# Kernel optimization log

Hardware: AMD Instinct MI355X
Metric: run time of the kernel (lower is better)

The kernel has to match this reference:

```python
import jax, jax.numpy as jnp
import numpy as np

B, T, D, H, L, W = 32, 512, 256, 8, 2, 10
NQ = 10000
HD = D // H


def setup_inputs():
    key = jax.random.key(0)
    ks = jax.random.split(key, 16)
    def n(k, shape, s=0.02):
        return jax.random.normal(k, shape, jnp.float32) * s
    return {
        "q": jax.random.randint(ks[0], (B, T), 0, NQ),
        "s": jax.random.randint(ks[1], (B, T), 0, 2),
        "q_embed": n(ks[2], (NQ + 1, D)),
        "s_embed": n(ks[3], (2, D)),
        "pos_embed": n(ks[4], (512, D)),
        "fusion_w": n(ks[5], (2 * D, D)),
        "fusion_b": jnp.zeros((D,), jnp.float32),
        "in_proj_w": n(ks[6], (L, D, 3 * D)),
        "in_proj_b": jnp.zeros((L, 3 * D), jnp.float32),
        "out_proj_w": n(ks[7], (L, D, D)),
        "out_proj_b": jnp.zeros((L, D), jnp.float32),
        "ln1_g": jnp.ones((L, D), jnp.float32),
        "ln1_b": jnp.zeros((L, D), jnp.float32),
        "ln2_g": jnp.ones((L, D), jnp.float32),
        "ln2_b": jnp.zeros((L, D), jnp.float32),
        "ff1_w": n(ks[8], (L, D, 4 * D)),
        "ff1_b": jnp.zeros((L, 4 * D), jnp.float32),
        "ff2_w": n(ks[9], (L, 4 * D, D)),
        "ff2_b": jnp.zeros((L, D), jnp.float32),
        "sw1": n(ks[10], (6, 32), 0.1),
        "sb1": jnp.zeros((32,), jnp.float32),
        "sw2": n(ks[11], (32, D // 4), 0.1),
        "sb2": jnp.zeros((D // 4,), jnp.float32),
        "cw1": n(ks[12], (D + D // 4, D)),
        "cb1": jnp.zeros((D,), jnp.float32),
        "cw2": n(ks[13], (D, 1)),
        "cb2": jnp.zeros((1,), jnp.float32),
    }


def _ln(x, g, b):
    mu = jnp.mean(x, -1, keepdims=True)
    var = jnp.mean(jnp.square(x - mu), -1, keepdims=True)
    return (x - mu) * jax.lax.rsqrt(var + 1e-5) * g + b


def _sliding_sum(x, w):
    # sum over trailing window of size w ending at each t, via prefix sums
    c = jnp.concatenate([jnp.zeros((x.shape[0], 1), x.dtype), jnp.cumsum(x, axis=1)], axis=1)
    t = jnp.arange(x.shape[1])
    return c[:, t + 1] - c[:, jnp.maximum(t + 1 - w, 0)]


def _stats(s, mask):
    # vectorized version of _extract_statistics (prefix-sum sliding windows)
    mf = mask.astype(jnp.float32)
    sf = s.astype(jnp.float32) * mf
    valid = _sliding_sum(mf, W)
    correct_rate = _sliding_sum(sf, W) / (valid + 1e-6)
    rc = _sliding_sum(mf, 5)
    recent_correct = _sliding_sum(sf, 5) / (rc + 1e-6)
    trans = ((s[:, 1:] != s[:, :-1]) & mask[:, 1:] & mask[:, :-1]).astype(jnp.float32)
    diff = jnp.concatenate([jnp.zeros((s.shape[0], 1), jnp.float32), trans], axis=1)
    change_rate = _sliding_sum(diff, W - 1) / (valid + 1e-6)
    # max consecutive equal run within each trailing window of size W
    sp = jnp.pad(s, ((0, 0), (W - 1, 0)))
    mp = jnp.pad(mask, ((0, 0), (W - 1, 0)))
    win_s = [sp[:, j:j + T] for j in range(W)]
    win_m = [mp[:, j:j + T] for j in range(W)]
    run = win_m[0].astype(jnp.float32)
    mx = run
    for j in range(1, W):  # fixed small window, not a data-dim loop
        eq = (win_s[j] == win_s[j - 1]) & win_m[j - 1]
        run = win_m[j].astype(jnp.float32) * (jnp.where(eq, run, 0.0) + 1.0)
        mx = jnp.maximum(mx, run)
    rel = jnp.broadcast_to(jnp.arange(T, dtype=jnp.float32) / max(T, 100), s.shape)
    cov = valid / W
    return jnp.stack([correct_rate, recent_correct, change_rate, mx / W, rel, cov], axis=-1)


def reference(q, s, q_embed, s_embed, pos_embed, fusion_w, fusion_b, in_proj_w, in_proj_b,
              out_proj_w, out_proj_b, ln1_g, ln1_b, ln2_g, ln2_b, ff1_w, ff1_b, ff2_w, ff2_b,
              sw1, sb1, sw2, sb2, cw1, cb1, cw2, cb2):
    mask = s >= 0
    qm = jnp.where(mask, q, 0)
    sm = jnp.where(mask, s, 0)
    h = jnp.concatenate([q_embed[qm], s_embed[sm]], axis=-1)  # [B,T,2D]
    h = jax.nn.relu(h @ fusion_w + fusion_b) + pos_embed[:T][None]
    causal = jnp.tril(jnp.ones((T, T), bool))
    allowed = causal[None, None] & mask[:, None, None, :]
    scale = 1.0 / (HD ** 0.5)
    for l in range(L):
        qkv = h @ in_proj_w[l] + in_proj_b[l]
        qh, kh, vh = jnp.split(qkv, 3, axis=-1)
        qh = qh.reshape(B, T, H, HD).transpose(0, 2, 1, 3)
        kh = kh.reshape(B, T, H, HD).transpose(0, 2, 1, 3)
        vh = vh.reshape(B, T, H, HD).transpose(0, 2, 1, 3)
        scores = jnp.einsum('bhqd,bhkd->bhqk', qh, kh) * scale
        scores = jnp.where(allowed, scores, -1e9)
        attn = jax.nn.softmax(scores, axis=-1)
        o = jnp.einsum('bhqk,bhkd->bhqd', attn, vh).transpose(0, 2, 1, 3).reshape(B, T, D)
        h = _ln(h + (o @ out_proj_w[l] + out_proj_b[l]), ln1_g[l], ln1_b[l])
        ff = jax.nn.gelu(h @ ff1_w[l] + ff1_b[l], approximate=False) @ ff2_w[l] + ff2_b[l]
        h = _ln(h + ff, ln2_g[l], ln2_b[l])
    sfeat = _stats(sm, mask)  # [B,T,6]
    semb = jax.nn.relu(sfeat @ sw1 + sb1) @ sw2 + sb2  # [B,T,D//4]
    comb = jnp.concatenate([h, semb], axis=-1)
    logits = (jax.nn.relu(comb @ cw1 + cb1) @ cw2 + cb2)[..., 0]
    return jnp.where(mask, logits, -1e9)
```

## Files before the change

kernel.cpp:

```cpp
#include <hip/hip_runtime.h>
#include <hip/hip_bf16.h>
#include <cmath>


using short8 = __attribute__((ext_vector_type(8))) short;
using short4v = __attribute__((ext_vector_type(4))) short;
using f32x4  = __attribute__((ext_vector_type(4))) float;

__device__ inline float gelu_f(float x) {
    return 0.5f * x * (1.0f + erff(x * 0.70710678118654752f));
}

__device__ inline short f2bf(float x) {
    union { float f; unsigned u; } v; v.f = x;
    return (short)((v.u + 0x7fffu + ((v.u >> 16) & 1u)) >> 16);
}

__device__ inline float bf2f(short v) {
    union { unsigned u; float f; } x; x.u = ((unsigned)(unsigned short)v) << 16;
    return x.f;
}

__device__ inline unsigned packbf(float lo, float hi) {
    union { float f; unsigned u; } a, b; a.f = lo; b.f = hi;
    unsigned ra = (a.u + 0x7fffu + ((a.u >> 16) & 1u)) >> 16;
    unsigned rb = (b.u + 0x7fffu + ((b.u >> 16) & 1u)) >> 16;
    return (rb << 16) | (ra & 0xffffu);
}

#define GLOAD16(gp, lp) __builtin_amdgcn_global_load_lds( \
    (const __attribute__((address_space(1))) void*)(gp), \
    (__attribute__((address_space(3))) void*)(lp), 16, 0, 0)

__global__ __launch_bounds__(256) void prep(
    const float* __restrict__ fusion_w, const float* __restrict__ in_proj_w,
    const float* __restrict__ out_proj_w, const float* __restrict__ ff1_w,
    const float* __restrict__ ff2_w, const float* __restrict__ cw1,
    short* __restrict__ wts,
    const int* __restrict__ s,
    short* __restrict__ semb,
    const float* __restrict__ sw1, const float* __restrict__ sb1,
    const float* __restrict__ sw2, const float* __restrict__ sb2)
{
    __shared__ float tile[32][33];
    __shared__ float sv_sh[512];
    __shared__ float m_sh[512];
    __shared__ float sw2_sh[2048];

    if (blockIdx.x < 1744) {
        const int b0[10]      = {0,128,320,512,576,640,896,1152,1408,1664};
        const int Ks[10]      = {512,256,256,256,256,256,256,1024,1024,320};
        const int Ns[10]      = {256,768,768,256,256,1024,1024,256,256,256};
        const int sidx[10]    = {0,1,1,2,2,3,3,4,4,5};
        const size_t soff[10] = {0,0,196608,0,65536,0,262144,0,262144,0};
        const size_t doff[10] = {0,131072,327680,524288,589824,655360,917504,1179648,1441792,1703936};
        const float* srcs[6] = {fusion_w, in_proj_w, out_proj_w, ff1_w, ff2_w, cw1};
        int bid = blockIdx.x;
        int mi = 0;
        while (mi < 9 && bid >= b0[mi + 1]) ++mi;
        int bl = bid - b0[mi];
        int K = Ks[mi], N = Ns[mi];
        int tx = bl % (N >> 5), ty = bl / (N >> 5);
        const float* src = srcs[sidx[mi]] + soff[mi];
        short* dst = wts + doff[mi];
        int c = threadIdx.x & 31, r = threadIdx.x >> 5;
#pragma unroll
        for (int i = 0; i < 4; ++i)
            tile[r + i * 8][c] = src[(size_t)(ty * 32 + r + i * 8) * N + tx * 32 + c];
        __syncthreads();
#pragma unroll
        for (int i = 0; i < 4; ++i)
            dst[(size_t)(tx * 32 + r + i * 8) * K + ty * 32 + c] = f2bf(tile[c][r + i * 8]);
    } else {
        const int b = blockIdx.x - 1744;
        const int tt = threadIdx.x;
        for (int t = tt; t < 512; t += 256) {
            int sval = s[b * 512 + t];
            bool mk = sval >= 0;
            sv_sh[t] = mk ? (float)sval : 0.f;
            m_sh[t] = mk ? 1.f : 0.f;
        }
        for (int i = tt; i < 2048; i += 256) sw2_sh[i] = sw2[i];
        __syncthreads();
        for (int half = 0; half < 2; ++half) {
            const int t = tt + half * 256;
            float mf10 = 0, sf10 = 0, mf5 = 0, sf5 = 0, d9 = 0;
#pragma unroll
            for (int k = 0; k < 10; ++k) {
                int idx = t - k;
                if (idx >= 0) {
                    float mv = m_sh[idx], sv = sv_sh[idx];
                    mf10 += mv; sf10 += sv;
                    if (k < 5) { mf5 += mv; sf5 += sv; }
                    if (k < 9 && idx >= 1) {
                        if (sv != sv_sh[idx - 1] && mv > 0.5f && m_sh[idx - 1] > 0.5f) d9 += 1.f;
                    }
                }
            }
            float run, mx;
            {
                int x0 = t - 9;
                run = (x0 >= 0) ? m_sh[x0] : 0.f;
                mx = run;
#pragma unroll
                for (int j = 1; j < 10; ++j) {
                    int xc = t + j - 9, xp = xc - 1;
                    float sc = (xc >= 0) ? sv_sh[xc] : 0.f;
                    float sp = (xp >= 0) ? sv_sh[xp] : 0.f;
                    float mc = (xc >= 0) ? m_sh[xc] : 0.f;
                    float mp = (xp >= 0) ? m_sh[xp] : 0.f;
                    bool eq = (sc == sp) && (mp > 0.5f);
                    run = (mc > 0.5f) ? ((eq ? run : 0.f) + 1.f) : 0.f;
                    mx = fmaxf(mx, run);
                }
            }
            float f[6];
            f[0] = sf10 / (mf10 + 1e-6f);
            f[1] = sf5 / (mf5 + 1e-6f);
            f[2] = d9 / (mf10 + 1e-6f);
            f[3] = mx * 0.1f;
            f[4] = (float)t * (1.f / 512.f);
            f[5] = mf10 * 0.1f;

            float hid[32];
#pragma unroll
            for (int j2 = 0; j2 < 32; ++j2) {
                float a = sb1[j2];
#pragma unroll
                for (int i = 0; i < 6; ++i) a = fmaf(f[i], sw1[i * 32 + j2], a);
                hid[j2] = fmaxf(a, 0.f);
            }
            short* orow = semb + ((size_t)b * 512 + t) * 64;
            for (int c = 0; c < 64; c += 4) {
                float v0 = sb2[c], v1 = sb2[c + 1], v2 = sb2[c + 2], v3 = sb2[c + 3];
#pragma unroll
                for (int j2 = 0; j2 < 32; ++j2) {
                    float hh = hid[j2];
                    v0 = fmaf(hh, sw2_sh[j2 * 64 + c], v0);
                    v1 = fmaf(hh, sw2_sh[j2 * 64 + c + 1], v1);
                    v2 = fmaf(hh, sw2_sh[j2 * 64 + c + 2], v2);
                    v3 = fmaf(hh, sw2_sh[j2 * 64 + c + 3], v3);
                }
                short4v o; o[0] = f2bf(v0); o[1] = f2bf(v1); o[2] = f2bf(v2); o[3] = f2bf(v3);
                *(short4v*)(orow + c) = o;
            }
        }
    }
}

template<int EPI, int KTOT>
__global__ __launch_bounds__(512) void kbs(
    const short* __restrict__ A, const short* __restrict__ Wt,
    const float* __restrict__ bias,
    short* __restrict__ o0, short* __restrict__ o1, short* __restrict__ o2,
    const float* __restrict__ pos,
    const int* __restrict__ qi, const int* __restrict__ si,
    const float* __restrict__ qe, const float* __restrict__ se)
{
    constexpr int BN = 64;
    constexpr int NCH = (KTOT + 255) / 256;
    __shared__ short Bs[BN * 256];
    const int tid = threadIdx.x, lane = tid & 63, wv = tid >> 6;
    const int lg = lane >> 4, lr = lane & 15;
    const int n0 = blockIdx.y * BN;
    const int row0 = blockIdx.x * 128 + wv * 16;

    f32x4 acc[4] = {};
    short8 af[8];

#pragma unroll
    for (int c = 0; c < NCH; ++c) {
        const int ck = (KTOT - c * 256 >= 256) ? 256 : (KTOT - c * 256);
        const int spr = ck >> 3;
        if (c) __syncthreads();
        for (int i = 0; i < (BN * ck) / 8; i += 512) {
            int slot = i + tid;
            int n = slot / spr, posn = slot % spr;
            int g = posn ^ (n & 7);
            GLOAD16(Wt + (size_t)(n0 + n) * KTOT + c * 256 + g * 8, &Bs[slot * 8]);
        }
        const int nkk = ck >> 5;
        if constexpr (EPI == 0) {
            int row = row0 + lr;
            int sv = si[row];
            bool mk = sv >= 0;
            const float* base = (c == 0) ? qe + (size_t)(mk ? qi[row] : 0) * 256
                                         : se + (size_t)(mk ? sv : 0) * 256;
#pragma unroll
            for (int kk = 0; kk < 8; ++kk) {
                const float* p = base + kk * 32 + lg * 8;
                float4 v0 = *(const float4*)p;
                float4 v1 = *(const float4*)(p + 4);
                short8 o;
                o[0] = f2bf(v0.x); o[1] = f2bf(v0.y); o[2] = f2bf(v0.z); o[3] = f2bf(v0.w);
                o[4] = f2bf(v1.x); o[5] = f2bf(v1.y); o[6] = f2bf(v1.z); o[7] = f2bf(v1.w);
                af[kk] = o;
            }
        } else {
            const short* ar = A + (size_t)(row0 + lr) * KTOT + c * 256 + lg * 8;
#pragma unroll
            for (int kk = 0; kk < 8; ++kk)
                if (kk < nkk) af[kk] = *(const short8*)(ar + kk * 32);
        }
        __syncthreads();
#pragma unroll
        for (int kk = 0; kk < 8; ++kk) {
            if (kk >= nkk) break;
#pragma unroll
            for (int j = 0; j < 4; ++j) {
                int n = j * 16 + lr;
                short8 b = *(const short8*)&Bs[n * ck + (((kk * 4 + lg) ^ (n & 7)) << 3)];
                acc[j] = __builtin_amdgcn_mfma_f32_16x16x32_bf16(af[kk], b, acc[j], 0, 0, 0);
            }
        }
    }

    if constexpr (EPI == 0) {
#pragma unroll
        for (int j = 0; j < 4; ++j)
#pragma unroll
        for (int r = 0; r < 4; ++r) {
            int row = row0 + lg * 4 + r;
            int col = n0 + j * 16 + lr;
            float x = acc[j][r] + bias[col];
            x = fmaxf(x, 0.f) + pos[(size_t)(row & 511) * 256 + col];
            o0[(size_t)row * 256 + col] = f2bf(x);
        }
    } else if constexpr (EPI == 1) {
#pragma unroll
        for (int j = 0; j < 4; ++j)
#pragma unroll
        for (int r = 0; r < 4; ++r) {
            int row = row0 + lg * 4 + r;
            int gcol = n0 + j * 16 + lr;
            int t = row & 511, bg = row >> 9;
            int sec = gcol >> 8, cc = gcol & 255;
            int h = cc >> 5, d = cc & 31, bh = bg * 8 + h;
            short v = f2bf(acc[j][r] + bias[gcol]);
            if (sec == 0)      o0[((size_t)bh * 512 + t) * 32 + d] = v;
            else if (sec == 1) o1[((size_t)bh * 512 + t) * 32 + d] = v;
            else {
                int kl = t & 31;
                o2[(size_t)bh * 16384 + (size_t)(t >> 5) * 1024 +
                   (size_t)((kl >> 2) & 3) * 256 + d * 8 + (((kl & 3) << 1) | ((kl >> 4) & 1))] = v;
            }
        }
    } else {
#pragma unroll
        for (int j = 0; j < 4; ++j)
#pragma unroll
        for (int r = 0; r < 4; ++r) {
            int row = row0 + lg * 4 + r;
            int gcol = n0 + j * 16 + lr;
            float x = acc[j][r] + bias[gcol];
            o0[(size_t)row * 1024 + gcol] = f2bf(gelu_f(x));
        }
    }
}

template<int EPI, int KTOT>
__global__ __launch_bounds__(512) void kfull(
    const short* __restrict__ A, const short* __restrict__ A2,
    const short* __restrict__ Wt, const float* __restrict__ bias,
    short* __restrict__ hb,
    const float* __restrict__ gamma, const float* __restrict__ beta,
    const float* __restrict__ cw2v, const float* __restrict__ cb2,
    const int* __restrict__ smask, float* __restrict__ outlog)
{
    constexpr int NCH = (KTOT + 127) / 128;
    constexpr int KA = (EPI == 1) ? 256 : KTOT;
    __shared__ short Bs[256 * 128];
    __shared__ float redS[32][4];
    __shared__ float redQ[32][4];
    const int tid = threadIdx.x, lane = tid & 63, wv = tid >> 6;
    const int lg = lane >> 4, lr = lane & 15;
    const int wr = wv >> 2, wc = wv & 3;
    const int row0 = blockIdx.x * 32 + wr * 16;

    f32x4 acc[4] = {};
    short8 af[4];

#pragma unroll
    for (int c = 0; c < NCH; ++c) {
        const int ck = (KTOT - c * 128 >= 128) ? 128 : (KTOT - c * 128);
        const int spr = ck >> 3;
        if (c) __syncthreads();
        for (int i = 0; i < (256 * ck) / 8; i += 512) {
            int slot = i + tid;
            int n = slot / spr, posn = slot % spr;
            int g = posn ^ (n & 7);
            GLOAD16(Wt + (size_t)n * KTOT + c * 128 + g * 8, &Bs[slot * 8]);
        }
        const int nkk = ck >> 5;
        if (EPI == 1 && c == 2) {
            const short* ar2 = A2 + (size_t)(row0 + lr) * 64 + lg * 8;
            af[0] = *(const short8*)(ar2);
            af[1] = *(const short8*)(ar2 + 32);
        } else {
            const short* ar = A + (size_t)(row0 + lr) * KA + c * 128 + lg * 8;
#pragma unroll
            for (int kk = 0; kk < 4; ++kk)
                if (kk < nkk) af[kk] = *(const short8*)(ar + kk * 32);
        }
        __syncthreads();
#pragma unroll
        for (int kk = 0; kk < 4; ++kk) {
            if (kk >= nkk) break;
#pragma unroll
            for (int j = 0; j < 4; ++j) {
                int n = wc * 64 + j * 16 + lr;
                short8 b = *(const short8*)&Bs[n * ck + (((kk * 4 + lg) ^ (n & 7)) << 3)];
                acc[j] = __builtin_amdgcn_mfma_f32_16x16x32_bf16(af[kk], b, acc[j], 0, 0, 0);
            }
        }
    }

    if constexpr (EPI == 0) {
        float ps[4] = {0.f, 0.f, 0.f, 0.f}, pq[4] = {0.f, 0.f, 0.f, 0.f};
#pragma unroll
        for (int j = 0; j < 4; ++j)
#pragma unroll
        for (int r = 0; r < 4; ++r) {
            int row = row0 + lg * 4 + r;
            int col = wc * 64 + j * 16 + lr;
            float x = acc[j][r] + bias[col] + bf2f(hb[(size_t)row * 256 + col]);
            acc[j][r] = x;
            ps[r] += x; pq[r] += x * x;
        }
#pragma unroll
        for (int off = 1; off < 16; off <<= 1)
#pragma unroll
            for (int r = 0; r < 4; ++r) {
                ps[r] += __shfl_xor(ps[r], off);
                pq[r] += __shfl_xor(pq[r], off);
            }
        if (lr == 0) {
#pragma unroll
            for (int r = 0; r < 4; ++r) {
                int rl = wr * 16 + lg * 4 + r;
                redS[rl][wc] = ps[r]; redQ[rl][wc] = pq[r];
            }
        }
        __syncthreads();
#pragma unroll
        for (int r = 0; r < 4; ++r) {
            int rl = wr * 16 + lg * 4 + r;
            int row = row0 + lg * 4 + r;
            float sm = redS[rl][0] + redS[rl][1] + redS[rl][2] + redS[rl][3];
            float sq = redQ[rl][0] + redQ[rl][1] + redQ[rl][2] + redQ[rl][3];
            float mu = sm * (1.f / 256.f);
            float var = sq * (1.f / 256.f) - mu * mu;
            float rstd = rsqrtf(var + 1e-5f);
#pragma unroll
            for (int j = 0; j < 4; ++j) {
                int col = wc * 64 + j * 16 + lr;
                float y = (acc[j][r] - mu) * rstd * gamma[col] + beta[col];
                hb[(size_t)row * 256 + col] = f2bf(y);
            }
        }
    } else {
        float p[4] = {0.f, 0.f, 0.f, 0.f};
#pragma unroll
        for (int j = 0; j < 4; ++j)
#pragma unroll
        for (int r = 0; r < 4; ++r) {
            int col = wc * 64 + j * 16 + lr;
            float v = fmaxf(acc[j][r] + bias[col], 0.f);
            p[r] += v * cw2v[col];
        }
#pragma unroll
        for (int off = 1; off < 16; off <<= 1)
#pragma unroll
            for (int r = 0; r < 4; ++r) p[r] += __shfl_xor(p[r], off);
        if (lr == 0) {
#pragma unroll
            for (int r = 0; r < 4; ++r)
                redS[wr * 16 + lg * 4 + r][wc] = p[r];
        }
        __syncthreads();
        if (tid < 32) {
            int row = blockIdx.x * 32 + tid;
            float v = redS[tid][0] + redS[tid][1] + redS[tid][2] + redS[tid][3] + cb2[0];
            outlog[row] = (smask[row] >= 0) ? v : -1e9f;
        }
    }
}

__global__ __launch_bounds__(256) void attn_mfma(
    const short* __restrict__ Qg, const short* __restrict__ Kg,
    const short* __restrict__ VTg, short* __restrict__ O)
{
    __shared__ unsigned Wp[4][2][16][20];
    const int bh = blockIdx.x >> 2, part = blockIdx.x & 3;
    const int b = bh >> 3, h = bh & 7;
    const int wv = threadIdx.x >> 6, lane = threadIdx.x & 63;
    const int lg = lane >> 4, lr = lane & 15;
    const int slot = part * 4 + wv;
    const short* Qbh = Qg + (size_t)bh * 16384;
    const short* Kbh = Kg + (size_t)bh * 16384;
    const short* Vbh = VTg + (size_t)bh * 16384;
    const float scale = 0.17677669529663687f;

    const int tA = slot, tB = 31 - slot;
    const int qA0 = tA << 4, qB0 = tB << 4;
    const int nA = tA >> 1, nB = tB >> 1;
    short8 qaA = *(const short8*)(Qbh + (size_t)(qA0 + lr) * 32 + lg * 8);
    short8 qaB = *(const short8*)(Qbh + (size_t)(qB0 + lr) * 32 + lg * 8);
    f32x4 oA0 = {}, oA1 = {}, oB0 = {}, oB1 = {};
    float lA[4] = {0.f, 0.f, 0.f, 0.f};
    float lB[4] = {0.f, 0.f, 0.f, 0.f};

    auto chunk = [&](int c, int q0, int nfull, const short8& qa,
                     const short8& kf0, const short8& kf1,
                     const short8& vf0, const short8& vf1,
                     f32x4& o0, f32x4& o1, float* l_, int slab) {
        int kc = c << 5;
        f32x4 s0 = {}, s1 = {};
        s0 = __builtin_amdgcn_mfma_f32_16x16x32_bf16(qa, kf0, s0, 0, 0, 0);
        s1 = __builtin_amdgcn_mfma_f32_16x16x32_bf16(qa, kf1, s1, 0, 0, 0);
        float p0[4], p1[4];
        if (c < nfull) {
#pragma unroll
            for (int r = 0; r < 4; ++r) {
                p0[r] = __expf(s0[r] * scale);
                p1[r] = __expf(s1[r] * scale);
            }
        } else {
#pragma unroll
            for (int r = 0; r < 4; ++r) {
                int qq = q0 + lg * 4 + r;
                p0[r] = (kc + lr)      > qq ? 0.f : __expf(s0[r] * scale);
                p1[r] = (kc + 16 + lr) > qq ? 0.f : __expf(s1[r] * scale);
            }
        }
#pragma unroll
        for (int r = 0; r < 4; ++r) {
            l_[r] += p0[r] + p1[r];
            Wp[wv][slab][lg * 4 + r][lr] = packbf(p0[r], p1[r]);
        }
        short8 pa = *(const short8*)&Wp[wv][slab][lr][lg * 4];
        o0 = __builtin_amdgcn_mfma_f32_16x16x32_bf16(pa, vf0, o0, 0, 0, 0);
        o1 = __builtin_amdgcn_mfma_f32_16x16x32_bf16(pa, vf1, o1, 0, 0, 0);
    };

    int c = 0;
    for (; c <= nA; ++c) {
        int kc = c << 5;
        short8 kf0 = *(const short8*)(Kbh + (size_t)(kc + lr) * 32 + lg * 8);
        short8 kf1 = *(const short8*)(Kbh + (size_t)(kc + 16 + lr) * 32 + lg * 8);
        short8 vf0 = *(const short8*)(Vbh + (size_t)c * 1024 + lg * 256 + lr * 8);
        short8 vf1 = *(const short8*)(Vbh + (size_t)c * 1024 + lg * 256 + (lr + 16) * 8);
        chunk(c, qB0, nB, qaB, kf0, kf1, vf0, vf1, oB0, oB1, lB, 1);
        chunk(c, qA0, nA, qaA, kf0, kf1, vf0, vf1, oA0, oA1, lA, 0);
    }
    for (; c <= nB; ++c) {
        int kc = c << 5;
        short8 kf0 = *(const short8*)(Kbh + (size_t)(kc + lr) * 32 + lg * 8);
        short8 kf1 = *(const short8*)(Kbh + (size_t)(kc + 16 + lr) * 32 + lg * 8);
        short8 vf0 = *(const short8*)(Vbh + (size_t)c * 1024 + lg * 256 + lr * 8);
        short8 vf1 = *(const short8*)(Vbh + (size_t)c * 1024 + lg * 256 + (lr + 16) * 8);
        chunk(c, qB0, nB, qaB, kf0, kf1, vf0, vf1, oB0, oB1, lB, 1);
    }

#pragma unroll
    for (int off = 1; off < 16; off <<= 1)
#pragma unroll
        for (int r = 0; r < 4; ++r) {
            lA[r] += __shfl_xor(lA[r], off);
            lB[r] += __shfl_xor(lB[r], off);
        }
#pragma unroll
    for (int r = 0; r < 4; ++r) {
        float invA = 1.f / lA[r];
        size_t roA = ((size_t)b * 512 + qA0 + lg * 4 + r) * 256 + h * 32;
        O[roA + lr] = f2bf(oA0[r] * invA);
        O[roA + 16 + lr] = f2bf(oA1[r] * invA);
        float invB = 1.f / lB[r];
        size_t roB = ((size_t)b * 512 + qB0 + lg * 4 + r) * 256 + h * 32;
        O[roB + lr] = f2bf(oB0[r] * invB);
        O[roB + 16 + lr] = f2bf(oB1[r] * invB);
    }
}

extern "C" void kernel_launch(void* const* d_in, const int* in_sizes, int n_in,
                              void* d_out, int out_size, void* d_ws, size_t ws_size,
                              hipStream_t stream) {
    const int*   q         = (const int*)d_in[0];
    const int*   s         = (const int*)d_in[1];
    const float* q_embed   = (const float*)d_in[2];
    const float* s_embed   = (const float*)d_in[3];
    const float* pos_embed = (const float*)d_in[4];
    const float* fusion_w  = (const float*)d_in[5];
    const float* fusion_b  = (const float*)d_in[6];
    const float* in_proj_w = (const float*)d_in[7];
    const float* in_proj_b = (const float*)d_in[8];
    const float* out_proj_w= (const float*)d_in[9];
    const float* out_proj_b= (const float*)d_in[10];
    const float* ln1_g     = (const float*)d_in[11];
    const float* ln1_b     = (const float*)d_in[12];
    const float* ln2_g     = (const float*)d_in[13];
    const float* ln2_b     = (const float*)d_in[14];
    const float* ff1_w     = (const float*)d_in[15];
    const float* ff1_b     = (const float*)d_in[16];
    const float* ff2_w     = (const float*)d_in[17];
    const float* ff2_b     = (const float*)d_in[18];
    const float* sw1       = (const float*)d_in[19];
    const float* sb1       = (const float*)d_in[20];
    const float* sw2       = (const float*)d_in[21];
    const float* sb2       = (const float*)d_in[22];
    const float* cw1       = (const float*)d_in[23];
    const float* cb1       = (const float*)d_in[24];
    const float* cw2       = (const float*)d_in[25];
    const float* cb2       = (const float*)d_in[26];
    float* out = (float*)d_out;

    char* base = (char*)d_ws;
    short* hb   = (short*)(base);
    short* bufA = (short*)(base + 8388608);
    short* att  = (short*)(base + 41943040);
    short* Qg   = (short*)(base + 50331648);
    short* Kg   = (short*)(base + 58720256);
    short* VTg  = (short*)(base + 67108864);
    short* semb = (short*)(base + 75497472);
    short* wts  = (short*)(base + 77594624);

    const size_t W_FUSION = 0, W_INPROJ0 = 131072, W_INPROJ1 = 327680;
    const size_t W_OUTPROJ0 = 524288, W_OUTPROJ1 = 589824;
    const size_t W_FF1_0 = 655360, W_FF1_1 = 917504;
    const size_t W_FF2_0 = 1179648, W_FF2_1 = 1441792;
    const size_t W_CW1 = 1703936;

    prep<<<1776, 256, 0, stream>>>(fusion_w, in_proj_w, out_proj_w,
                                   ff1_w, ff2_w, cw1, wts,
                                   s, semb, sw1, sb1, sw2, sb2);
    kbs<0, 512><<<dim3(128, 4), 512, 0, stream>>>(nullptr,
        wts + W_FUSION, fusion_b, hb, nullptr, nullptr,
        pos_embed, q, s, q_embed, s_embed);
    for (int l = 0; l < 2; ++l) {
        kbs<1, 256><<<dim3(128, 12), 512, 0, stream>>>(hb,
            wts + (l ? W_INPROJ1 : W_INPROJ0), in_proj_b + l * 768,
            Qg, Kg, VTg, nullptr, nullptr, nullptr, nullptr, nullptr);
        attn_mfma<<<1024, 256, 0, stream>>>(Qg, Kg, VTg, att);
        kfull<0, 256><<<512, 512, 0, stream>>>(att, nullptr,
            wts + (l ? W_OUTPROJ1 : W_OUTPROJ0), out_proj_b + l * 256,
            hb, ln1_g + l * 256, ln1_b + l * 256,
            nullptr, nullptr, nullptr, nullptr);
        kbs<2, 256><<<dim3(128, 16), 512, 0, stream>>>(hb,
            wts + (l ? W_FF1_1 : W_FF1_0), ff1_b + l * 1024,
            bufA, nullptr, nullptr, nullptr, nullptr, nullptr, nullptr, nullptr);
        kfull<0, 1024><<<512, 512, 0, stream>>>(bufA, nullptr,
            wts + (l ? W_FF2_1 : W_FF2_0), ff2_b + l * 256,
            hb, ln2_g + l * 256, ln2_b + l * 256,
            nullptr, nullptr, nullptr, nullptr);
    }
    kfull<1, 320><<<512, 512, 0, stream>>>(hb, semb,
        wts + W_CW1, cb1, nullptr, nullptr, nullptr,
        cw2, cb2, s, out);
}
```

Measured before the change: 280.8 us.

## Reuse weight tile across multiple M sub-tiles and double-buffer attention P staging

The kbs GEMM now loads the full-K weight slice into LDS once and loops over MS row sub-tiles, halving the grid for the QKV and FF1 projections. This amortises the weight loads across more rows, at the cost of larger LDS use (64xKTOT, which is 64 KB for the 512-wide fusion GEMM) and fewer blocks. In attention, exp is switched to exp2 with a prescaled log2e constant, and the P staging buffer is split by chunk parity to reduce the write-after-read hazard between iterations.

New measurement: 290.3 us. 3.4% more time.

```diff
diff --git a/kernel.cpp b/kernel.cpp
--- a/kernel.cpp
+++ b/kernel.cpp
@@ -148,7 +148,7 @@
     }
 }
 
-template<int EPI, int KTOT>
+template<int EPI, int KTOT, int MS>
 __global__ __launch_bounds__(512) void kbs(
     const short* __restrict__ A, const short* __restrict__ Wt,
     const float* __restrict__ bias,
@@ -158,37 +158,35 @@
     const float* __restrict__ qe, const float* __restrict__ se)
 {
     constexpr int BN = 64;
-    constexpr int NCH = (KTOT + 255) / 256;
-    __shared__ short Bs[BN * 256];
+    constexpr int SPR = KTOT / 8;
+    constexpr int NK = KTOT / 32;
+    __shared__ short Bs[BN * KTOT];
     const int tid = threadIdx.x, lane = tid & 63, wv = tid >> 6;
     const int lg = lane >> 4, lr = lane & 15;
     const int n0 = blockIdx.y * BN;
-    const int row0 = blockIdx.x * 128 + wv * 16;
-
-    f32x4 acc[4] = {};
-    short8 af[8];
-
-#pragma unroll
-    for (int c = 0; c < NCH; ++c) {
-        const int ck = (KTOT - c * 256 >= 256) ? 256 : (KTOT - c * 256);
-        const int spr = ck >> 3;
-        if (c) __syncthreads();
-        for (int i = 0; i < (BN * ck) / 8; i += 512) {
-            int slot = i + tid;
-            int n = slot / spr, posn = slot % spr;
-            int g = posn ^ (n & 7);
-            GLOAD16(Wt + (size_t)(n0 + n) * KTOT + c * 256 + g * 8, &Bs[slot * 8]);
-        }
-        const int nkk = ck >> 5;
+
+#pragma unroll
+    for (int i = 0; i < (BN * SPR) / 512; ++i) {
+        int slot = i * 512 + tid;
+        int n = slot / SPR, posn = slot % SPR;
+        int g = posn ^ (n & 7);
+        GLOAD16(Wt + (size_t)(n0 + n) * KTOT + g * 8, &Bs[slot * 8]);
+    }
+    __syncthreads();
+
+#pragma unroll
+    for (int m = 0; m < MS; ++m) {
+        const int row0 = (blockIdx.x * MS + m) * 128 + wv * 16;
+        short8 af[NK];
         if constexpr (EPI == 0) {
             int row = row0 + lr;
             int sv = si[row];
             bool mk = sv >= 0;
-            const float* base = (c == 0) ? qe + (size_t)(mk ? qi[row] : 0) * 256
-                                         : se + (size_t)(mk ? sv : 0) * 256;
-#pragma unroll
-            for (int kk = 0; kk < 8; ++kk) {
-                const float* p = base + kk * 32 + lg * 8;
+            const float* b0 = qe + (size_t)(mk ? qi[row] : 0) * 256;
+            const float* b1 = se + (size_t)(mk ? sv : 0) * 256;
+#pragma unroll
+            for (int kk = 0; kk < NK; ++kk) {
+                const float* p = ((kk < 8) ? b0 + kk * 32 : b1 + (kk - 8) * 32) + lg * 8;
                 float4 v0 = *(const float4*)p;
                 float4 v1 = *(const float4*)(p + 4);
                 short8 o;
@@ -197,63 +195,63 @@
                 af[kk] = o;
             }
         } else {
-            const short* ar = A + (size_t)(row0 + lr) * KTOT + c * 256 + lg * 8;
-#pragma unroll
-            for (int kk = 0; kk < 8; ++kk)
-                if (kk < nkk) af[kk] = *(const short8*)(ar + kk * 32);
-        }
-        __syncthreads();
-#pragma unroll
-        for (int kk = 0; kk < 8; ++kk) {
-            if (kk >= nkk) break;
+            const short* ar = A + (size_t)(row0 + lr) * KTOT + lg * 8;
+#pragma unroll
+            for (int kk = 0; kk < NK; ++kk)
+                af[kk] = *(const short8*)(ar + kk * 32);
+        }
+
+        f32x4 acc[4] = {};
+#pragma unroll
+        for (int kk = 0; kk < NK; ++kk) {
 #pragma unroll
             for (int j = 0; j < 4; ++j) {
                 int n = j * 16 + lr;
-                short8 b = *(const short8*)&Bs[n * ck + (((kk * 4 + lg) ^ (n & 7)) << 3)];
+                short8 b = *(const short8*)&Bs[n * KTOT + (((kk * 4 + lg) ^ (n & 7)) << 3)];
                 acc[j] = __builtin_amdgcn_mfma_f32_16x16x32_bf16(af[kk], b, acc[j], 0, 0, 0);
             }
         }
-    }
-
-    if constexpr (EPI == 0) {
-#pragma unroll
-        for (int j = 0; j < 4; ++j)
-#pragma unroll
-        for (int r = 0; r < 4; ++r) {
-            int row = row0 + lg * 4 + r;
-            int col = n0 + j * 16 + lr;
-            float x = acc[j][r] + bias[col];
-            x = fmaxf(x, 0.f) + pos[(size_t)(row & 511) * 256 + col];
-            o0[(size_t)row * 256 + col] = f2bf(x);
-        }
-    } else if constexpr (EPI == 1) {
-#pragma unroll
-        for (int j = 0; j < 4; ++j)
-#pragma unroll
-        for (int r = 0; r < 4; ++r) {
-            int row = row0 + lg * 4 + r;
-            int gcol = n0 + j * 16 + lr;
-            int t = row & 511, bg = row >> 9;
-            int sec = gcol >> 8, cc = gcol & 255;
-            int h = cc >> 5, d = cc & 31, bh = bg * 8 + h;
-            short v = f2bf(acc[j][r] + bias[gcol]);
-            if (sec == 0)      o0[((size_t)bh * 512 + t) * 32 + d] = v;
-            else if (sec == 1) o1[((size_t)bh * 512 + t) * 32 + d] = v;
-            else {
-                int kl = t & 31;
-                o2[(size_t)bh * 16384 + (size_t)(t >> 5) * 1024 +
-                   (size_t)((kl >> 2) & 3) * 256 + d * 8 + (((kl & 3) << 1) | ((kl >> 4) & 1))] = v;
-            }
-        }
-    } else {
-#pragma unroll
-        for (int j = 0; j < 4; ++j)
-#pragma unroll
-        for (int r = 0; r < 4; ++r) {
-            int row = row0 + lg * 4 + r;
-            int gcol = n0 + j * 16 + lr;
-            float x = acc[j][r] + bias[gcol];
-            o0[(size_t)row * 1024 + gcol] = f2bf(gelu_f(x));
+
+        if constexpr (EPI == 0) {
+#pragma unroll
+            for (int j = 0; j < 4; ++j)
+#pragma unroll
+            for (int r = 0; r < 4; ++r) {
+                int row = row0 + lg * 4 + r;
+                int col = n0 + j * 16 + lr;
+                float x = acc[j][r] + bias[col];
+                x = fmaxf(x, 0.f) + pos[(size_t)(row & 511) * 256 + col];
+                o0[(size_t)row * 256 + col] = f2bf(x);
+            }
+        } else if constexpr (EPI == 1) {
+#pragma unroll
+            for (int j = 0; j < 4; ++j)
+#pragma unroll
+            for (int r = 0; r < 4; ++r) {
+                int row = row0 + lg * 4 + r;
+                int gcol = n0 + j * 16 + lr;
+                int t = row & 511, bg = row >> 9;
+                int sec = gcol >> 8, cc = gcol & 255;
+                int h = cc >> 5, d = cc & 31, bh = bg * 8 + h;
+                short v = f2bf(acc[j][r] + bias[gcol]);
+                if (sec == 0)      o0[((size_t)bh * 512 + t) * 32 + d] = v;
+                else if (sec == 1) o1[((size_t)bh * 512 + t) * 32 + d] = v;
+                else {
+                    int kl = t & 31;
+                    o2[(size_t)bh * 16384 + (size_t)(t >> 5) * 1024 +
+                       (size_t)((kl >> 2) & 3) * 256 + d * 8 + (((kl & 3) << 1) | ((kl >> 4) & 1))] = v;
+                }
+            }
+        } else {
+#pragma unroll
+            for (int j = 0; j < 4; ++j)
+#pragma unroll
+            for (int r = 0; r < 4; ++r) {
+                int row = row0 + lg * 4 + r;
+                int gcol = n0 + j * 16 + lr;
+                float x = acc[j][r] + bias[gcol];
+                o0[(size_t)row * 1024 + gcol] = f2bf(gelu_f(x));
+            }
         }
     }
 }
@@ -390,7 +388,7 @@
     const short* __restrict__ Qg, const short* __restrict__ Kg,
     const short* __restrict__ VTg, short* __restrict__ O)
 {
-    __shared__ unsigned Wp[4][2][16][20];
+    __shared__ unsigned Wp[4][2][2][16][20];
     const int bh = blockIdx.x >> 2, part = blockIdx.x & 3;
     const int b = bh >> 3, h = bh & 7;
     const int wv = threadIdx.x >> 6, lane = threadIdx.x & 63;
@@ -399,7 +397,7 @@
     const short* Qbh = Qg + (size_t)bh * 16384;
     const short* Kbh = Kg + (size_t)bh * 16384;
     const short* Vbh = VTg + (size_t)bh * 16384;
-    const float scale = 0.17677669529663687f;
+    const float cs = 0.25503590f;
 
     const int tA = slot, tB = 31 - slot;
     const int qA0 = tA << 4, qB0 = tB << 4;
@@ -415,6 +413,7 @@
                      const short8& vf0, const short8& vf1,
                      f32x4& o0, f32x4& o1, float* l_, int slab) {
         int kc = c << 5;
+        int par = c & 1;
         f32x4 s0 = {}, s1 = {};
         s0 = __builtin_amdgcn_mfma_f32_16x16x32_bf16(qa, kf0, s0, 0, 0, 0);
         s1 = __builtin_amdgcn_mfma_f32_16x16x32_bf16(qa, kf1, s1, 0, 0, 0);
@@ -422,23 +421,23 @@
         if (c < nfull) {
 #pragma unroll
             for (int r = 0; r < 4; ++r) {
-                p0[r] = __expf(s0[r] * scale);
-                p1[r] = __expf(s1[r] * scale);
+                p0[r] = exp2f(s0[r] * cs);
+                p1[r] = exp2f(s1[r] * cs);
             }
         } else {
 #pragma unroll
             for (int r = 0; r < 4; ++r) {
                 int qq = q0 + lg * 4 + r;
-                p0[r] = (kc + lr)      > qq ? 0.f : __expf(s0[r] * scale);
-                p1[r] = (kc + 16 + lr) > qq ? 0.f : __expf(s1[r] * scale);
+                p0[r] = (kc + lr)      > qq ? 0.f : exp2f(s0[r] * cs);
+                p1[r] = (kc + 16 + lr) > qq ? 0.f : exp2f(s1[r] * cs);
             }
         }
 #pragma unroll
         for (int r = 0; r < 4; ++r) {
             l_[r] += p0[r] + p1[r];
-            Wp[wv][slab][lg * 4 + r][lr] = packbf(p0[r], p1[r]);
-        }
-        short8 pa = *(const short8*)&Wp[wv][slab][lr][lg * 4];
+            Wp[wv][slab][par][lg * 4 + r][lr] = packbf(p0[r], p1[r]);
+        }
+        short8 pa = *(const short8*)&Wp[wv][slab][par][lr][lg * 4];
         o0 = __builtin_amdgcn_mfma_f32_16x16x32_bf16(pa, vf0, o0, 0, 0, 0);
         o1 = __builtin_amdgcn_mfma_f32_16x16x32_bf16(pa, vf1, o1, 0, 0, 0);
     };
@@ -533,11 +532,11 @@
     prep<<<1776, 256, 0, stream>>>(fusion_w, in_proj_w, out_proj_w,
                                    ff1_w, ff2_w, cw1, wts,
                                    s, semb, sw1, sb1, sw2, sb2);
-    kbs<0, 512><<<dim3(128, 4), 512, 0, stream>>>(nullptr,
+    kbs<0, 512, 1><<<dim3(128, 4), 512, 0, stream>>>(nullptr,
         wts + W_FUSION, fusion_b, hb, nullptr, nullptr,
         pos_embed, q, s, q_embed, s_embed);
     for (int l = 0; l < 2; ++l) {
-        kbs<1, 256><<<dim3(128, 12), 512, 0, stream>>>(hb,
+        kbs<1, 256, 2><<<dim3(64, 12), 512, 0, stream>>>(hb,
             wts + (l ? W_INPROJ1 : W_INPROJ0), in_proj_b + l * 768,
             Qg, Kg, VTg, nullptr, nullptr, nullptr, nullptr, nullptr);
         attn_mfma<<<1024, 256, 0, stream>>>(Qg, Kg, VTg, att);
@@ -545,7 +544,7 @@
             wts + (l ? W_OUTPROJ1 : W_OUTPROJ0), out_proj_b + l * 256,
             hb, ln1_g + l * 256, ln1_b + l * 256,
             nullptr, nullptr, nullptr, nullptr);
-        kbs<2, 256><<<dim3(128, 16), 512, 0, stream>>>(hb,
+        kbs<2, 256, 2><<<dim3(64, 16), 512, 0, stream>>>(hb,
             wts + (l ? W_FF1_1 : W_FF1_0), ff1_b + l * 1024,
             bufA, nullptr, nullptr, nullptr, nullptr, nullptr, nullptr, nullptr);
         kfull<0, 1024><<<512, 512, 0, stream>>>(bufA, nullptr,
```
